# Kernel optimization log

Hardware: AMD Instinct MI355X
Metric: run time of the kernel (lower is better)

The kernel has to match this reference:

```python
import jax, jax.numpy as jnp
import numpy as np

INPUT_SIZE = 2048
HIDDEN_SIZE = 4096
NUM_CLASSES = 1000
BATCH = 4096


def setup_inputs() -> dict:
    key = jax.random.key(0)
    kx, k1, k2, k3 = jax.random.split(key, 4)
    x = jax.random.normal(kx, (BATCH, INPUT_SIZE), dtype=jnp.float32)
    w1 = jax.random.normal(k1, (INPUT_SIZE, HIDDEN_SIZE), dtype=jnp.float32) * 0.01
    b1 = jnp.zeros((HIDDEN_SIZE,), dtype=jnp.float32)
    w2 = jax.random.normal(k2, (HIDDEN_SIZE, HIDDEN_SIZE), dtype=jnp.float32) * 0.01
    b2 = jnp.zeros((HIDDEN_SIZE,), dtype=jnp.float32)
    w3 = jax.random.normal(k3, (HIDDEN_SIZE, NUM_CLASSES), dtype=jnp.float32) * 0.01
    b3 = jnp.zeros((NUM_CLASSES,), dtype=jnp.float32)
    return {"x": x, "w1": w1, "b1": b1, "w2": w2, "b2": b2, "w3": w3, "b3": b3}


def reference(x, w1, b1, w2, b2, w3, b3):
    # fused GEMM + bias + ReLU, equivalent to the original Python double-loop matmul
    h1 = jax.nn.relu(x @ w1 + b1)    # [B, H]
    h2 = jax.nn.relu(h1 @ w2 + b2)   # [B, H]
    out = h2 @ w3 + b3               # [B, C]
    return out
```

## Files before the change

kernel.cpp:

```cpp
#include <hip/hip_runtime.h>
#include <hip/hip_bf16.h>

typedef __bf16 bf16x8 __attribute__((ext_vector_type(8)));
typedef __bf16 bf16x4 __attribute__((ext_vector_type(4)));
typedef float floatx4 __attribute__((ext_vector_type(4)));

#define B_    4096
#define IN_   2048
#define HID_  4096
#define NC_   1000
#define NCP_  1024

__device__ __forceinline__ void transpose_cvt_dev(const float* __restrict__ src,
                                                  __bf16* __restrict__ dst,
                                                  int R, int C, int bx, int by,
                                                  float* tile ) {
    const int r0 = bx * 64;
    const int c0 = by * 64;
    const int t  = threadIdx.x;
#pragma unroll
    for (int it = 0; it < 4; ++it) {
        int lin = it * 256 + t;
        int sr = lin >> 4, c4 = lin & 15;
        int cb = c0 + c4 * 4;
        const float* s = src + (size_t)(r0 + sr) * C;
        float4 v;
        if (cb + 3 < C) {
            v = *(const float4*)(s + cb);
        } else {
            v.x = (cb + 0 < C) ? s[cb + 0] : 0.f;
            v.y = (cb + 1 < C) ? s[cb + 1] : 0.f;
            v.z = (cb + 2 < C) ? s[cb + 2] : 0.f;
            v.w = (cb + 3 < C) ? s[cb + 3] : 0.f;
        }
        tile[(c4 * 4 + 0) * 65 + sr] = v.x;
        tile[(c4 * 4 + 1) * 65 + sr] = v.y;
        tile[(c4 * 4 + 2) * 65 + sr] = v.z;
        tile[(c4 * 4 + 3) * 65 + sr] = v.w;
    }
    __syncthreads();
#pragma unroll
    for (int it = 0; it < 2; ++it) {
        int lin = it * 256 + t;
        int dr = lin >> 3, q8 = lin & 7;
        bf16x8 o;
#pragma unroll
        for (int j = 0; j < 8; ++j) o[j] = (__bf16)tile[dr * 65 + q8 * 8 + j];
        *(bf16x8*)(dst + (size_t)(c0 + dr) * R + r0 + q8 * 8) = o;
    }
}

__device__ __forceinline__ void swizzle32x32(int bid, int& bx, int& by) {
    int xcd = bid & 7;
    int q   = bid >> 3;
    by = ((xcd >> 2) << 4) + (q & 15);
    bx = ((xcd & 3) << 3) + (q >> 4);
}

template <bool RELU, bool OUT_BF16>
__device__ __forceinline__ void gemm_core(const __bf16* __restrict__ A,
                                          const __bf16* __restrict__ Bt,
                                          const float* __restrict__ bias,
                                          void* __restrict__ Cv,
                                          int M, int K, int Nstore,
                                          int bx, int by,
                                          __bf16* sA, __bf16* sB) {
    const int tid   = threadIdx.x;
    const int lane  = tid & 63;
    const int wave  = tid >> 6;
    const int wr    = wave >> 1;
    const int wc    = wave & 1;
    const int mBase = by * 128;
    const int nBase = bx * 128;
    const int lr    = lane >> 4;
    const int lc    = lane & 15;

    floatx4 acc[4][4];
#pragma unroll
    for (int i = 0; i < 4; ++i)
#pragma unroll
        for (int j = 0; j < 4; ++j) acc[i][j] = (floatx4)0.f;

    for (int k0 = 0; k0 < K; k0 += 64) {
#pragma unroll
        for (int it = 0; it < 4; ++it) {
            int lin = it * 256 + tid;
            int r   = lin >> 3;
            int kc  = (lin & 7) ^ (r & 7);
            const __bf16* ga = A  + (size_t)(mBase + r) * K + k0 + kc * 8;
            const __bf16* gb = Bt + (size_t)(nBase + r) * K + k0 + kc * 8;
            __builtin_amdgcn_global_load_lds(
                (__attribute__((address_space(1))) void*)ga,
                (__attribute__((address_space(3))) void*)(sA + lin * 8), 16, 0, 0);
            __builtin_amdgcn_global_load_lds(
                (__attribute__((address_space(1))) void*)gb,
                (__attribute__((address_space(3))) void*)(sB + lin * 8), 16, 0, 0);
        }
        __builtin_amdgcn_s_waitcnt(0);
        __syncthreads();

#pragma unroll
        for (int kk = 0; kk < 2; ++kk) {
            const int sw = (kk * 4 + lr) ^ (lc & 7);
            bf16x8 af[4], bfr[4];
#pragma unroll
            for (int i = 0; i < 4; ++i)
                af[i] = *(const bf16x8*)(sA + (wr * 64 + i * 16 + lc) * 64 + sw * 8);
#pragma unroll
            for (int j = 0; j < 4; ++j)
                bfr[j] = *(const bf16x8*)(sB + (wc * 64 + j * 16 + lc) * 64 + sw * 8);
#pragma unroll
            for (int i = 0; i < 4; ++i)
#pragma unroll
                for (int j = 0; j < 4; ++j)
                    acc[i][j] = __builtin_amdgcn_mfma_f32_16x16x32_bf16(af[i], bfr[j], acc[i][j], 0, 0, 0);
        }
        __syncthreads();
    }

#pragma unroll
    for (int j = 0; j < 4; ++j) {
        int col = nBase + wc * 64 + j * 16 + lc;
        if (col < Nstore) {
            float bv = bias[col];
#pragma unroll
            for (int i = 0; i < 4; ++i) {
                int rowb = mBase + wr * 64 + i * 16 + lr * 4;
#pragma unroll
                for (int r = 0; r < 4; ++r) {
                    float v = acc[i][j][r] + bv;
                    if (RELU) v = fmaxf(v, 0.f);
                    if (OUT_BF16)
                        ((__bf16*)Cv)[(size_t)(rowb + r) * Nstore + col] = (__bf16)v;
                    else
                        ((float*)Cv)[(size_t)(rowb + r) * Nstore + col] = v;
                }
            }
        }
    }
}

__global__ __launch_bounds__(256) void prep1(const float* __restrict__ x,
                                             __bf16* __restrict__ xb,
                                             const float* __restrict__ w1,
                                             __bf16* __restrict__ w1t) {
    __shared__ float tile[64 * 65];
    const int b = blockIdx.x;
    if (b < 4096) {
        int i = (b * 256 + (int)threadIdx.x) * 8;
        float4 a = *(const float4*)(x + i);
        float4 c = *(const float4*)(x + i + 4);
        bf16x8 o;
        o[0] = (__bf16)a.x; o[1] = (__bf16)a.y; o[2] = (__bf16)a.z; o[3] = (__bf16)a.w;
        o[4] = (__bf16)c.x; o[5] = (__bf16)c.y; o[6] = (__bf16)c.z; o[7] = (__bf16)c.w;
        *(bf16x8*)(xb + i) = o;
    } else {
        int l = b - 4096;
        transpose_cvt_dev(w1, w1t, IN_, HID_, l & 31, l >> 5, tile);
    }
}

__global__ __launch_bounds__(256, 2) void gemm1_fused(const __bf16* __restrict__ xb,
                                                      const __bf16* __restrict__ w1t,
                                                      const float* __restrict__ b1,
                                                      __bf16* __restrict__ h1,
                                                      const float* __restrict__ w2,
                                                      __bf16* __restrict__ w2t,
                                                      const float* __restrict__ w3,
                                                      __bf16* __restrict__ w3t) {
    __shared__ float smem[8192];
    const int b = blockIdx.x;
    if (b < 1024) {
        __bf16* sA = (__bf16*)smem;
        __bf16* sB = sA + 128 * 64;
        int bx, by;
        swizzle32x32(b, bx, by);
        gemm_core<true, true>(xb, w1t, b1, h1, B_, IN_, HID_, bx, by, sA, sB);
    } else if (b < 5120) {
        int l = b - 1024;
        transpose_cvt_dev(w2, w2t, HID_, HID_, l & 63, l >> 6, smem);
    } else {
        int l = b - 5120;
        transpose_cvt_dev(w3, w3t, HID_, NC_, l & 63, l >> 6, smem);
    }
}

#define BAR() __builtin_amdgcn_s_barrier()
#define LGKM(n)                                                  \
    asm volatile("s_waitcnt lgkmcnt(" #n ")" ::: "memory");      \
    __builtin_amdgcn_sched_barrier(0)
#define VMCNT(n) asm volatile("s_waitcnt vmcnt(" #n ")" ::: "memory")

#define LDA2(dst, mb, pA)                                                      \
    _Pragma("unroll") for (int mi_ = 0; mi_ < 2; ++mi_)                        \
    _Pragma("unroll") for (int kk_ = 0; kk_ < 2; ++kk_)                        \
        dst[mi_][kk_] = *(const bf16x8*)((pA) +                                \
            (wr * 128 + ((mb) + mi_) * 16 + lc) * 64 +                         \
            (((kk_ * 4) + lr) ^ (lc & 7)) * 8);

#define LDB8(pB)                                                               \
    _Pragma("unroll") for (int n_ = 0; n_ < 4; ++n_)                           \
    _Pragma("unroll") for (int kk_ = 0; kk_ < 2; ++kk_)                        \
        bq[n_][kk_] = *(const bf16x8*)((pB) +                                  \
            (wc * 64 + n_ * 16 + lc) * 64 +                                    \
            (((kk_ * 4) + lr) ^ (lc & 7)) * 8);

#define MFMA16(aset, mb)                                                       \
    _Pragma("unroll") for (int mi_ = 0; mi_ < 2; ++mi_)                        \
    _Pragma("unroll") for (int n_ = 0; n_ < 4; ++n_) {                         \
        acc[(mb) + mi_][n_] = __builtin_amdgcn_mfma_f32_16x16x32_bf16(         \
            aset[mi_][0], bq[n_][0], acc[(mb) + mi_][n_], 0, 0, 0);            \
        acc[(mb) + mi_][n_] = __builtin_amdgcn_mfma_f32_16x16x32_bf16(         \
            aset[mi_][1], bq[n_][1], acc[(mb) + mi_][n_], 0, 0, 0);            \
    }

#define DO_TILE(base, S0, S1, ...) {                                           \
    const __bf16* pA_ = (base);                                                \
    const __bf16* pB_ = (base) + 16384;                                        \
    bf16x8 bq[4][2], aX[2][2], aY[2][2];                                       \
    LDB8(pB_);                                                                 \
    LDA2(aX, 0, pA_);                                                          \
    LDA2(aY, 2, pA_);                                                          \
    S0;                                                                        \
    BAR(); LGKM(4);                                                            \
    __builtin_amdgcn_s_setprio(1); MFMA16(aX, 0); __builtin_amdgcn_s_setprio(0); \
    BAR();                                                                     \
    LDA2(aX, 4, pA_);                                                          \
    S1;                                                                        \
    BAR(); LGKM(4);                                                            \
    __builtin_amdgcn_s_setprio(1); MFMA16(aY, 2); __builtin_amdgcn_s_setprio(0); \
    BAR();                                                                     \
    LDA2(aY, 6, pA_);                                                          \
    BAR(); LGKM(4);                                                            \
    __builtin_amdgcn_s_setprio(1); MFMA16(aX, 4); __builtin_amdgcn_s_setprio(0); \
    BAR();                                                                     \
    LGKM(0);                                                                   \
    __builtin_amdgcn_s_setprio(1); MFMA16(aY, 6); __builtin_amdgcn_s_setprio(0); \
    BAR();                                                                     \
    __VA_ARGS__;                                                               \
    BAR();                                                                     \
}

__global__ __launch_bounds__(512, 2) void gemm2_256(const __bf16* __restrict__ A,
                                                    const __bf16* __restrict__ Bt,
                                                    const float* __restrict__ bias,
                                                    __bf16* __restrict__ C) {
    extern __shared__ __bf16 lds[];
    const int NT = HID_ / 64;

    const int tid  = threadIdx.x;
    const int lane = tid & 63;
    const int wave = tid >> 6;
    const int wr   = wave >> 2;
    const int wc   = wave & 3;
    const int lr   = lane >> 4;
    const int lc   = lane & 15;

    int bid = blockIdx.y * 16 + blockIdx.x;
    int xcd = bid & 7, q = bid >> 3;
    const int by = (xcd & 3) * 4 + (q & 3);
    const int bx = (xcd >> 2) * 8 + (q >> 2);
    const int mBase = by * 256;
    const int nBase = bx * 256;

    auto stage_half = [&](const __bf16* __restrict__ src, int rowBase, int k0,
                          __bf16* dst) {
#pragma unroll
        for (int it = 0; it < 2; ++it) {
            int lin = it * 512 + tid;
            int rl  = lin >> 3;
            int kc  = (lin & 7) ^ (rl & 7);
            const __bf16* gp = src + (size_t)(rowBase + rl) * HID_ + k0 + kc * 8;
            __builtin_amdgcn_global_load_lds(
                (__attribute__((address_space(1))) void*)gp,
                (__attribute__((address_space(3))) void*)(dst + lin * 8), 16, 0, 0);
        }
    };

    floatx4 acc[8][4];
#pragma unroll
    for (int i = 0; i < 8; ++i)
#pragma unroll
        for (int j = 0; j < 4; ++j) acc[i][j] = (floatx4)0.f;

    stage_half(A,  mBase,       0,  lds);
    stage_half(A,  mBase + 128, 0,  lds + 8192);
    stage_half(Bt, nBase,       0,  lds + 16384);
    stage_half(Bt, nBase + 128, 0,  lds + 16384 + 8192);
    stage_half(A,  mBase,       64, lds + 32768);
    stage_half(A,  mBase + 128, 64, lds + 32768 + 8192);
    VMCNT(4);
    BAR();

    for (int t = 0; t < NT; t += 2) {
        DO_TILE(lds,
                stage_half(Bt, nBase,       (t + 1) * 64, lds + 49152),
                stage_half(Bt, nBase + 128, (t + 1) * 64, lds + 49152 + 8192),
                if (t + 2 < NT) {
                    stage_half(A, mBase,       (t + 2) * 64, lds);
                    stage_half(A, mBase + 128, (t + 2) * 64, lds + 8192);
                    VMCNT(4);
                } else {
                    VMCNT(0);
                });
        DO_TILE(lds + 32768,
                if (t + 2 < NT) stage_half(Bt, nBase,       (t + 2) * 64, lds + 16384),
                if (t + 2 < NT) stage_half(Bt, nBase + 128, (t + 2) * 64, lds + 16384 + 8192),
                if (t + 3 < NT) {
                    stage_half(A, mBase,       (t + 3) * 64, lds + 32768);
                    stage_half(A, mBase + 128, (t + 3) * 64, lds + 32768 + 8192);
                    VMCNT(4);
                } else {
                    VMCNT(0);
                });
    }

#pragma unroll
    for (int n = 0; n < 4; ++n) {
        int col = nBase + wc * 64 + n * 16 + lc;
        float bv = bias[col];
#pragma unroll
        for (int m = 0; m < 8; ++m) {
            int rowb = mBase + wr * 128 + m * 16 + lr * 4;
#pragma unroll
            for (int r = 0; r < 4; ++r) {
                float v = fmaxf(acc[m][n][r] + bv, 0.f);
                C[(size_t)(rowb + r) * HID_ + col] = (__bf16)v;
            }
        }
    }
}

__global__ __launch_bounds__(256, 2) void gemm_sk(const __bf16* __restrict__ A,
                                                  const __bf16* __restrict__ Bt,
                                                  float* __restrict__ P,
                                                  int M, int KH, int Ktot) {
    __shared__ __bf16 sA[128 * 64];
    __shared__ __bf16 sB[128 * 64];

    const int tid   = threadIdx.x;
    const int lane  = tid & 63;
    const int wave  = tid >> 6;
    const int wr    = wave >> 1;
    const int wc    = wave & 1;
    const int mBase = blockIdx.y * 128;
    const int nBase = blockIdx.x * 128;
    const int z     = blockIdx.z;
    const int kOff  = z * KH;
    const int lr    = lane >> 4;
    const int lc    = lane & 15;

    floatx4 acc[4][4];
#pragma unroll
    for (int i = 0; i < 4; ++i)
#pragma unroll
        for (int j = 0; j < 4; ++j) acc[i][j] = (floatx4)0.f;

    for (int k0 = kOff; k0 < kOff + KH; k0 += 64) {
#pragma unroll
        for (int it = 0; it < 4; ++it) {
            int lin = it * 256 + tid;
            int r   = lin >> 3;
            int kc  = (lin & 7) ^ (r & 7);
            const __bf16* ga = A  + (size_t)(mBase + r) * Ktot + k0 + kc * 8;
            const __bf16* gb = Bt + (size_t)(nBase + r) * Ktot + k0 + kc * 8;
            __builtin_amdgcn_global_load_lds(
                (__attribute__((address_space(1))) void*)ga,
                (__attribute__((address_space(3))) void*)(sA + lin * 8), 16, 0, 0);
            __builtin_amdgcn_global_load_lds(
                (__attribute__((address_space(1))) void*)gb,
                (__attribute__((address_space(3))) void*)(sB + lin * 8), 16, 0, 0);
        }
        __builtin_amdgcn_s_waitcnt(0);
        __syncthreads();

#pragma unroll
        for (int kk = 0; kk < 2; ++kk) {
            const int sw = (kk * 4 + lr) ^ (lc & 7);
            bf16x8 af[4], bfr[4];
#pragma unroll
            for (int i = 0; i < 4; ++i)
                af[i] = *(const bf16x8*)(sA + (wr * 64 + i * 16 + lc) * 64 + sw * 8);
#pragma unroll
            for (int j = 0; j < 4; ++j)
                bfr[j] = *(const bf16x8*)(sB + (wc * 64 + j * 16 + lc) * 64 + sw * 8);
#pragma unroll
            for (int i = 0; i < 4; ++i)
#pragma unroll
                for (int j = 0; j < 4; ++j)
                    acc[i][j] = __builtin_amdgcn_mfma_f32_16x16x32_bf16(af[i], bfr[j], acc[i][j], 0, 0, 0);
        }
        __syncthreads();
    }

    float* Pz = P + (size_t)z * M * NCP_;
#pragma unroll
    for (int j = 0; j < 4; ++j) {
        int col = nBase + wc * 64 + j * 16 + lc;
#pragma unroll
        for (int i = 0; i < 4; ++i) {
            int rowb = mBase + wr * 64 + i * 16 + lr * 4;
#pragma unroll
            for (int r = 0; r < 4; ++r)
                Pz[(size_t)(rowb + r) * NCP_ + col] = acc[i][j][r];
        }
    }
}

__global__ __launch_bounds__(256) void reduce_bias(const float* __restrict__ P,
                                                   const float* __restrict__ b3,
                                                   float* __restrict__ out) {
    int c = blockIdx.x * 256 + threadIdx.x;
    int m = blockIdx.y;
    if (c < NC_)
        out[(size_t)m * NC_ + c] =
            P[(size_t)m * NCP_ + c] + P[(size_t)(B_ + m) * NCP_ + c] + b3[c];
}

extern "C" void kernel_launch(void* const* d_in, const int* in_sizes, int n_in,
                              void* d_out, int out_size, void* d_ws, size_t ws_size,
                              hipStream_t stream) {
    const float* x  = (const float*)d_in[0];
    const float* w1 = (const float*)d_in[1];
    const float* b1 = (const float*)d_in[2];
    const float* w2 = (const float*)d_in[3];
    const float* b2 = (const float*)d_in[4];
    const float* w3 = (const float*)d_in[5];
    const float* b3 = (const float*)d_in[6];
    float* out = (float*)d_out;

    char* ws = (char*)d_ws;
    __bf16* xb  = (__bf16*)(ws);
    __bf16* w1t = (__bf16*)(ws + (16u << 20));
    __bf16* w2t = (__bf16*)(ws + (32u << 20));
    __bf16* w3t = (__bf16*)(ws + (64u << 20));
    __bf16* h1  = (__bf16*)(ws + (72u << 20));
    __bf16* h2  = (__bf16*)(ws);
    float*  P   = (float*)(ws + (72u << 20));

    static int attr_done = 0;
    if (!attr_done) {
        (void)hipFuncSetAttribute((const void*)gemm2_256,
                                  hipFuncAttributeMaxDynamicSharedMemorySize,
                                  131072);
        attr_done = 1;
    }

    prep1<<<6144, 256, 0, stream>>>(x, xb, w1, w1t);

    gemm1_fused<<<6144, 256, 0, stream>>>(xb, w1t, b1, h1, w2, w2t, w3, w3t);

    gemm2_256<<<dim3(16, 16), 512, 131072, stream>>>(h1, w2t, b2, h2);

    gemm_sk<<<dim3(NCP_ / 128, B_ / 128, 2), 256, 0, stream>>>(
        h2, w3t, P, B_, HID_ / 2, HID_);
    reduce_bias<<<dim3(NCP_ / 256, B_), 256, 0, stream>>>(P, b3, out);
}
```

Baseline: 428.8 us.

## Software-pipeline LDS fragment reads across k-tiles in middle GEMM

Restructures the hidden-layer GEMM main loop so B fragments and the first A fragment of the next k-tile are read from LDS during the last MFMA groups of the current tile, using double-buffered register sets. Whole A+B k-tiles are staged into alternating LDS halves after compute finishes, instead of splitting A and B staging across phases. The goal is to hide LDS read latency and reduce stalls at tile boundaries. The cost is more registers for two B fragment sets and coarser global-load waits (vmcnt(0) mid-tile), which could expose memory latency.

```diff
diff --git a/kernel.cpp b/kernel.cpp
--- a/kernel.cpp
+++ b/kernel.cpp
@@ -185,69 +185,79 @@
     }
 }
 
+#define PRIO1 __builtin_amdgcn_s_setprio(1)
+#define PRIO0 __builtin_amdgcn_s_setprio(0)
 #define BAR() __builtin_amdgcn_s_barrier()
 #define LGKM(n)                                                  \
     asm volatile("s_waitcnt lgkmcnt(" #n ")" ::: "memory");      \
     __builtin_amdgcn_sched_barrier(0)
 #define VMCNT(n) asm volatile("s_waitcnt vmcnt(" #n ")" ::: "memory")
 
-#define LDA2(dst, mb, pA)                                                      \
+#define RDA(dst, mp, base)                                                     \
     _Pragma("unroll") for (int mi_ = 0; mi_ < 2; ++mi_)                        \
     _Pragma("unroll") for (int kk_ = 0; kk_ < 2; ++kk_)                        \
-        dst[mi_][kk_] = *(const bf16x8*)((pA) +                                \
-            (wr * 128 + ((mb) + mi_) * 16 + lc) * 64 +                         \
-            (((kk_ * 4) + lr) ^ (lc & 7)) * 8);
-
-#define LDB8(pB)                                                               \
-    _Pragma("unroll") for (int n_ = 0; n_ < 4; ++n_)                           \
+        dst[mi_][kk_] = *(const bf16x8*)((base) +                              \
+            (wr * 128 + ((mp) * 2 + mi_) * 16 + lc) * 64 +                     \
+            ((kk_ * 4 + lr) ^ (lc & 7)) * 8);
+
+#define RDB2(dst, np, base)                                                    \
+    _Pragma("unroll") for (int j_ = 0; j_ < 2; ++j_)                           \
     _Pragma("unroll") for (int kk_ = 0; kk_ < 2; ++kk_)                        \
-        bq[n_][kk_] = *(const bf16x8*)((pB) +                                  \
-            (wc * 64 + n_ * 16 + lc) * 64 +                                    \
-            (((kk_ * 4) + lr) ^ (lc & 7)) * 8);
-
-#define MFMA16(aset, mb)                                                       \
+        dst[(np) * 2 + j_][kk_] = *(const bf16x8*)((base) + 16384 +            \
+            (wc * 64 + ((np) * 2 + j_) * 16 + lc) * 64 +                       \
+            ((kk_ * 4 + lr) ^ (lc & 7)) * 8);
+
+#define MFMA16(aset, mp, bset)                                                 \
     _Pragma("unroll") for (int mi_ = 0; mi_ < 2; ++mi_)                        \
     _Pragma("unroll") for (int n_ = 0; n_ < 4; ++n_) {                         \
-        acc[(mb) + mi_][n_] = __builtin_amdgcn_mfma_f32_16x16x32_bf16(         \
-            aset[mi_][0], bq[n_][0], acc[(mb) + mi_][n_], 0, 0, 0);            \
-        acc[(mb) + mi_][n_] = __builtin_amdgcn_mfma_f32_16x16x32_bf16(         \
-            aset[mi_][1], bq[n_][1], acc[(mb) + mi_][n_], 0, 0, 0);            \
-    }
-
-#define DO_TILE(base, S0, S1, ...) {                                           \
-    const __bf16* pA_ = (base);                                                \
-    const __bf16* pB_ = (base) + 16384;                                        \
-    bf16x8 bq[4][2], aX[2][2], aY[2][2];                                       \
-    LDB8(pB_);                                                                 \
-    LDA2(aX, 0, pA_);                                                          \
-    LDA2(aY, 2, pA_);                                                          \
-    S0;                                                                        \
-    BAR(); LGKM(4);                                                            \
-    __builtin_amdgcn_s_setprio(1); MFMA16(aX, 0); __builtin_amdgcn_s_setprio(0); \
-    BAR();                                                                     \
-    LDA2(aX, 4, pA_);                                                          \
-    S1;                                                                        \
-    BAR(); LGKM(4);                                                            \
-    __builtin_amdgcn_s_setprio(1); MFMA16(aY, 2); __builtin_amdgcn_s_setprio(0); \
-    BAR();                                                                     \
-    LDA2(aY, 6, pA_);                                                          \
-    BAR(); LGKM(4);                                                            \
-    __builtin_amdgcn_s_setprio(1); MFMA16(aX, 4); __builtin_amdgcn_s_setprio(0); \
-    BAR();                                                                     \
-    LGKM(0);                                                                   \
-    __builtin_amdgcn_s_setprio(1); MFMA16(aY, 6); __builtin_amdgcn_s_setprio(0); \
-    BAR();                                                                     \
-    __VA_ARGS__;                                                               \
-    BAR();                                                                     \
-}
+        acc[(mp) * 2 + mi_][n_] = __builtin_amdgcn_mfma_f32_16x16x32_bf16(     \
+            aset[mi_][0], bset[n_][0], acc[(mp) * 2 + mi_][n_], 0, 0, 0);      \
+        acc[(mp) * 2 + mi_][n_] = __builtin_amdgcn_mfma_f32_16x16x32_bf16(     \
+            aset[mi_][1], bset[n_][1], acc[(mp) * 2 + mi_][n_], 0, 0, 0);      \
+    }
+
+#define STAGE4(kt, base)                                                       \
+    stage_half(A,  mBase,       (kt) * 64, (base));                            \
+    stage_half(A,  mBase + 128, (kt) * 64, (base) + 8192);                     \
+    stage_half(Bt, nBase,       (kt) * 64, (base) + 16384);                    \
+    stage_half(Bt, nBase + 128, (kt) * 64, (base) + 24576);
+
+#define TILE_STEADY(CUR, NXT, bqC, bqN, kt2)                                   \
+     RDA(aV, 1, CUR);                                                  \
+    BAR(); LGKM(4); PRIO1; MFMA16(aU, 0, bqC); PRIO0; BAR();                   \
+     RDA(aU, 2, CUR);                                                  \
+    BAR(); LGKM(4); PRIO1; MFMA16(aV, 1, bqC); PRIO0; VMCNT(0); BAR();         \
+     RDA(aV, 3, CUR); RDB2(bqN, 0, NXT);                               \
+    BAR(); LGKM(8); PRIO1; MFMA16(aU, 2, bqC); PRIO0; BAR();                   \
+     RDA(aU, 0, NXT); RDB2(bqN, 1, NXT);                               \
+    BAR(); LGKM(12); PRIO1; MFMA16(aV, 3, bqC); PRIO0;                         \
+    STAGE4(kt2, CUR);                                                          \
+    BAR();
+
+#define TILE_DRAIN(CUR, NXT, bqC, bqN)                                         \
+    RDA(aV, 1, CUR);                                                           \
+    BAR(); LGKM(4); PRIO1; MFMA16(aU, 0, bqC); PRIO0; BAR();                   \
+    RDA(aU, 2, CUR);                                                           \
+    BAR(); LGKM(4); PRIO1; MFMA16(aV, 1, bqC); PRIO0; VMCNT(0); BAR();         \
+    RDA(aV, 3, CUR); RDB2(bqN, 0, NXT);                                        \
+    BAR(); LGKM(8); PRIO1; MFMA16(aU, 2, bqC); PRIO0; BAR();                   \
+    RDA(aU, 0, NXT); RDB2(bqN, 1, NXT);                                        \
+    BAR(); LGKM(12); PRIO1; MFMA16(aV, 3, bqC); PRIO0; BAR();
+
+#define TILE_LAST(CUR, bqC)                                                    \
+    RDA(aV, 1, CUR);                                                           \
+    BAR(); LGKM(4); PRIO1; MFMA16(aU, 0, bqC); PRIO0; BAR();                   \
+    RDA(aU, 2, CUR);                                                           \
+    BAR(); LGKM(4); PRIO1; MFMA16(aV, 1, bqC); PRIO0; BAR();                   \
+    RDA(aV, 3, CUR);                                                           \
+    BAR(); LGKM(4); PRIO1; MFMA16(aU, 2, bqC); PRIO0; BAR();                   \
+    LGKM(0); MFMA16(aV, 3, bqC);
 
 __global__ __launch_bounds__(512, 2) void gemm2_256(const __bf16* __restrict__ A,
                                                     const __bf16* __restrict__ Bt,
                                                     const float* __restrict__ bias,
                                                     __bf16* __restrict__ C) {
     extern __shared__ __bf16 lds[];
-    const int NT = HID_ / 64;
-
     const int tid  = threadIdx.x;
     const int lane = tid & 63;
     const int wave = tid >> 6;
@@ -262,6 +272,9 @@
     const int bx = (xcd >> 2) * 8 + (q >> 2);
     const int mBase = by * 256;
     const int nBase = bx * 256;
+
+    __bf16* const S0p = lds;
+    __bf16* const S1p = lds + 32768;
 
     auto stage_half = [&](const __bf16* __restrict__ src, int rowBase, int k0,
                           __bf16* dst) {
@@ -283,37 +296,23 @@
 #pragma unroll
         for (int j = 0; j < 4; ++j) acc[i][j] = (floatx4)0.f;
 
-    stage_half(A,  mBase,       0,  lds);
-    stage_half(A,  mBase + 128, 0,  lds + 8192);
-    stage_half(Bt, nBase,       0,  lds + 16384);
-    stage_half(Bt, nBase + 128, 0,  lds + 16384 + 8192);
-    stage_half(A,  mBase,       64, lds + 32768);
-    stage_half(A,  mBase + 128, 64, lds + 32768 + 8192);
-    VMCNT(4);
+    bf16x8 bqE[4][2], bqO[4][2];
+    bf16x8 aU[2][2], aV[2][2];
+
+    STAGE4(0, S0p);
+    STAGE4(1, S1p);
+    VMCNT(8);
     BAR();
-
-    for (int t = 0; t < NT; t += 2) {
-        DO_TILE(lds,
-                stage_half(Bt, nBase,       (t + 1) * 64, lds + 49152),
-                stage_half(Bt, nBase + 128, (t + 1) * 64, lds + 49152 + 8192),
-                if (t + 2 < NT) {
-                    stage_half(A, mBase,       (t + 2) * 64, lds);
-                    stage_half(A, mBase + 128, (t + 2) * 64, lds + 8192);
-                    VMCNT(4);
-                } else {
-                    VMCNT(0);
-                });
-        DO_TILE(lds + 32768,
-                if (t + 2 < NT) stage_half(Bt, nBase,       (t + 2) * 64, lds + 16384),
-                if (t + 2 < NT) stage_half(Bt, nBase + 128, (t + 2) * 64, lds + 16384 + 8192),
-                if (t + 3 < NT) {
-                    stage_half(A, mBase,       (t + 3) * 64, lds + 32768);
-                    stage_half(A, mBase + 128, (t + 3) * 64, lds + 32768 + 8192);
-                    VMCNT(4);
-                } else {
-                    VMCNT(0);
-                });
-    }
+    RDB2(bqE, 0, S0p);
+    RDB2(bqE, 1, S0p);
+    RDA(aU, 0, S0p);
+
+    for (int t = 0; t < 62; t += 2) {
+        TILE_STEADY(S0p, S1p, bqE, bqO, t + 2);
+        TILE_STEADY(S1p, S0p, bqO, bqE, t + 3);
+    }
+    TILE_DRAIN(S0p, S1p, bqE, bqO);
+    TILE_LAST(S1p, bqO);
 
 #pragma unroll
     for (int n = 0; n < 4; ++n) {
```

New measurement: 639.1 us. 49.0% more time.

## Restructure gemm2 pipeline into simple double-buffered full-tile prefetch

Applied to the files above, without the earlier changes.

Replaces the staggered A/B half-tile prefetch schedule in the 256x256 GEMM with a plain double buffer: each tile waits for all outstanding loads, then issues the full A and B stage for the next K-tile into the other buffer before its MFMAs. This simplifies the wait and barrier pattern and removes the trailing barriers per tile. The occupancy hint drops from 2 to 1 block per CU in launch_bounds, giving the compiler more registers. A full vmcnt(0) at each tile start may expose more load latency than the staggered scheme did.

```diff
diff --git a/kernel.cpp b/kernel.cpp
--- a/kernel.cpp
+++ b/kernel.cpp
@@ -185,6 +185,8 @@
     }
 }
 
+#define PRIO1 __builtin_amdgcn_s_setprio(1)
+#define PRIO0 __builtin_amdgcn_s_setprio(0)
 #define BAR() __builtin_amdgcn_s_barrier()
 #define LGKM(n)                                                  \
     asm volatile("s_waitcnt lgkmcnt(" #n ")" ::: "memory");      \
@@ -214,40 +216,50 @@
             aset[mi_][1], bq[n_][1], acc[(mb) + mi_][n_], 0, 0, 0);            \
     }
 
-#define DO_TILE(base, S0, S1, ...) {                                           \
-    const __bf16* pA_ = (base);                                                \
-    const __bf16* pB_ = (base) + 16384;                                        \
+#define STAGE4(kt, base)                                                       \
+    stage_half(A,  mBase,       (kt) * 64, (base));                            \
+    stage_half(A,  mBase + 128, (kt) * 64, (base) + 8192);                     \
+    stage_half(Bt, nBase,       (kt) * 64, (base) + 16384);                    \
+    stage_half(Bt, nBase + 128, (kt) * 64, (base) + 24576);
+
+#define TILE_S(CUR, OTH, ktS) {                                                \
+    VMCNT(0);                        \
+    BAR();                                         \
+    const __bf16* pA_ = (CUR);                                                 \
+    const __bf16* pB_ = (CUR) + 16384;                                         \
     bf16x8 bq[4][2], aX[2][2], aY[2][2];                                       \
-    LDB8(pB_);                                                                 \
-    LDA2(aX, 0, pA_);                                                          \
-    LDA2(aY, 2, pA_);                                                          \
-    S0;                                                                        \
-    BAR(); LGKM(4);                                                            \
-    __builtin_amdgcn_s_setprio(1); MFMA16(aX, 0); __builtin_amdgcn_s_setprio(0); \
+    LDB8(pB_); LDA2(aX, 0, pA_); LDA2(aY, 2, pA_);            \
+    STAGE4(ktS, OTH);                   \
+    LGKM(4);                                                                   \
+    PRIO1; MFMA16(aX, 0); PRIO0; BAR();                                        \
+    LDA2(aX, 4, pA_);                                                          \
+    BAR(); LGKM(4); PRIO1; MFMA16(aY, 2); PRIO0; BAR();                        \
+    LDA2(aY, 6, pA_);                                                          \
+    BAR(); LGKM(4); PRIO1; MFMA16(aX, 4); PRIO0; BAR();                        \
+    LGKM(0); PRIO1; MFMA16(aY, 6); PRIO0; BAR();      \
+}
+
+#define TILE_L(CUR) {                                                          \
+    VMCNT(0);                                                                  \
     BAR();                                                                     \
+    const __bf16* pA_ = (CUR);                                                 \
+    const __bf16* pB_ = (CUR) + 16384;                                         \
+    bf16x8 bq[4][2], aX[2][2], aY[2][2];                                       \
+    LDB8(pB_); LDA2(aX, 0, pA_); LDA2(aY, 2, pA_);                             \
+    LGKM(4);                                                                   \
+    PRIO1; MFMA16(aX, 0); PRIO0; BAR();                                        \
     LDA2(aX, 4, pA_);                                                          \
-    S1;                                                                        \
-    BAR(); LGKM(4);                                                            \
-    __builtin_amdgcn_s_setprio(1); MFMA16(aY, 2); __builtin_amdgcn_s_setprio(0); \
-    BAR();                                                                     \
+    BAR(); LGKM(4); PRIO1; MFMA16(aY, 2); PRIO0; BAR();                        \
     LDA2(aY, 6, pA_);                                                          \
-    BAR(); LGKM(4);                                                            \
-    __builtin_amdgcn_s_setprio(1); MFMA16(aX, 4); __builtin_amdgcn_s_setprio(0); \
-    BAR();                                                                     \
-    LGKM(0);                                                                   \
-    __builtin_amdgcn_s_setprio(1); MFMA16(aY, 6); __builtin_amdgcn_s_setprio(0); \
-    BAR();                                                                     \
-    __VA_ARGS__;                                                               \
-    BAR();                                                                     \
-}
-
-__global__ __launch_bounds__(512, 2) void gemm2_256(const __bf16* __restrict__ A,
+    BAR(); LGKM(4); PRIO1; MFMA16(aX, 4); PRIO0; BAR();                        \
+    LGKM(0); MFMA16(aY, 6);                                                    \
+}
+
+__global__ __launch_bounds__(512, 1) void gemm2_256(const __bf16* __restrict__ A,
                                                     const __bf16* __restrict__ Bt,
                                                     const float* __restrict__ bias,
                                                     __bf16* __restrict__ C) {
     extern __shared__ __bf16 lds[];
-    const int NT = HID_ / 64;
-
     const int tid  = threadIdx.x;
     const int lane = tid & 63;
     const int wave = tid >> 6;
@@ -262,6 +274,9 @@
     const int bx = (xcd >> 2) * 8 + (q >> 2);
     const int mBase = by * 256;
     const int nBase = bx * 256;
+
+    __bf16* const S0p = lds;
+    __bf16* const S1p = lds + 32768;
 
     auto stage_half = [&](const __bf16* __restrict__ src, int rowBase, int k0,
                           __bf16* dst) {
@@ -283,37 +298,14 @@
 #pragma unroll
         for (int j = 0; j < 4; ++j) acc[i][j] = (floatx4)0.f;
 
-    stage_half(A,  mBase,       0,  lds);
-    stage_half(A,  mBase + 128, 0,  lds + 8192);
-    stage_half(Bt, nBase,       0,  lds + 16384);
-    stage_half(Bt, nBase + 128, 0,  lds + 16384 + 8192);
-    stage_half(A,  mBase,       64, lds + 32768);
-    stage_half(A,  mBase + 128, 64, lds + 32768 + 8192);
-    VMCNT(4);
-    BAR();
-
-    for (int t = 0; t < NT; t += 2) {
-        DO_TILE(lds,
-                stage_half(Bt, nBase,       (t + 1) * 64, lds + 49152),
-                stage_half(Bt, nBase + 128, (t + 1) * 64, lds + 49152 + 8192),
-                if (t + 2 < NT) {
-                    stage_half(A, mBase,       (t + 2) * 64, lds);
-                    stage_half(A, mBase + 128, (t + 2) * 64, lds + 8192);
-                    VMCNT(4);
-                } else {
-                    VMCNT(0);
-                });
-        DO_TILE(lds + 32768,
-                if (t + 2 < NT) stage_half(Bt, nBase,       (t + 2) * 64, lds + 16384),
-                if (t + 2 < NT) stage_half(Bt, nBase + 128, (t + 2) * 64, lds + 16384 + 8192),
-                if (t + 3 < NT) {
-                    stage_half(A, mBase,       (t + 3) * 64, lds + 32768);
-                    stage_half(A, mBase + 128, (t + 3) * 64, lds + 32768 + 8192);
-                    VMCNT(4);
-                } else {
-                    VMCNT(0);
-                });
-    }
+    STAGE4(0, S0p);
+
+    for (int t = 0; t < 62; t += 2) {
+        TILE_S(S0p, S1p, t + 1);
+        TILE_S(S1p, S0p, t + 2);
+    }
+    TILE_S(S0p, S1p, 63);
+    TILE_L(S1p);
 
 #pragma unroll
     for (int n = 0; n < 4; ++n) {
```

New measurement: 424.7 us. About the same (-1.0%).
